# Performance work log

Hardware: AMD Instinct MI355X
Metric: run time of the kernel (lower is better)

Reference implementation:

```python
import jax, jax.numpy as jnp
from jax import lax
import numpy as np

V, E, H, L, B, ML, T = 32000, 512, 512, 2, 64, 64, 32


def setup_inputs() -> dict:
    key = jax.random.key(0)
    ks = jax.random.split(key, 16)
    s = 0.05
    return {
        "current_input": jax.random.randint(ks[0], (B,), 0, V),
        "h0": jax.random.normal(ks[1], (L, B, H), jnp.float32),
        "c0": jax.random.normal(ks[2], (L, B, H), jnp.float32),
        "encoder_output": jax.random.normal(ks[3], (ML, B, H), jnp.float32),
        "gtruth": jax.random.randint(ks[4], (T, B), 0, V),
        "length": T,
        "emb": s * jax.random.normal(ks[5], (V, E), jnp.float32),
        "attn_W": s * jax.random.normal(ks[6], (ML, E + H), jnp.float32),
        "attn_out_W": s * jax.random.normal(ks[7], (E, E + H), jnp.float32),
        "lstm_Wi": s * jax.random.normal(ks[8], (L, 4 * H, E), jnp.float32),
        "lstm_Wh": s * jax.random.normal(ks[9], (L, 4 * H, H), jnp.float32),
        "lstm_bi": s * jax.random.normal(ks[10], (L, 4 * H), jnp.float32),
        "lstm_bh": s * jax.random.normal(ks[11], (L, 4 * H), jnp.float32),
        "gen_W": s * jax.random.normal(ks[12], (V, H), jnp.float32),
        "gen_b": s * jax.random.normal(ks[13], (V,), jnp.float32),
    }


def _lstm_cell(x, h, c, Wi, Wh, bi, bh):
    # PyTorch gate order: i, f, g, o
    g = x @ Wi.T + h @ Wh.T + bi + bh  # [B, 4H]
    i, f, gg, o = jnp.split(g, 4, axis=-1)
    c_new = jax.nn.sigmoid(f) * c + jax.nn.sigmoid(i) * jnp.tanh(gg)
    h_new = jax.nn.sigmoid(o) * jnp.tanh(c_new)
    return h_new, c_new


def reference(current_input, h0, c0, encoder_output, gtruth, length,
              emb, attn_W, attn_out_W, lstm_Wi, lstm_Wh, lstm_bi, lstm_bh,
              gen_W, gen_b):
    n_layers = h0.shape[0]

    def step_fn(carry, tok):
        h, c = carry  # each [L, B, H]
        emb_t = emb[tok]                                   # [B, E]
        attn_in = jnp.concatenate([emb_t, h[-1]], axis=1)  # [B, E+H]
        a = jax.nn.softmax(attn_in @ attn_W.T, axis=1)     # [B, ML]
        ctx = jnp.einsum('bl,lbh->bh', a, encoder_output)  # [B, H]
        rnn_in = jax.nn.relu(
            jnp.concatenate([emb_t, ctx], axis=1) @ attn_out_W.T)  # [B, E]
        x = rnn_in
        hs, cs = [], []
        for l in range(n_layers):
            hn, cn = _lstm_cell(x, h[l], c[l], lstm_Wi[l], lstm_Wh[l],
                                lstm_bi[l], lstm_bh[l])
            hs.append(hn)
            cs.append(cn)
            x = hn
        scores = x @ gen_W.T + gen_b  # [B, V]
        return (jnp.stack(hs), jnp.stack(cs)), scores

    # teacher forcing: step t consumes current_input at t=0, gtruth[t-1] after
    tokens = jnp.concatenate([current_input[None], gtruth[:-1]], axis=0)  # [T, B]
    (h_fin, c_fin), outputs = lax.scan(step_fn, (h0, c0), tokens)
    return outputs, h_fin, c_fin
```

## Files before the change

kernel.cpp:

```cpp
#include <hip/hip_runtime.h>
#include <hip/hip_bf16.h>

typedef __bf16 bf16_t;
typedef bf16_t bf16x8 __attribute__((ext_vector_type(8)));
typedef bf16_t bf16x4 __attribute__((ext_vector_type(4)));
typedef float f32x4 __attribute__((ext_vector_type(4)));

#define MFMA(a, b, c) __builtin_amdgcn_mfma_f32_16x16x32_bf16((a), (b), (c), 0, 0, 0)

__device__ __forceinline__ float sigm(float x) { return 1.f / (1.f + __expf(-x)); }
__device__ __forceinline__ float tanh_f(float x) { return 1.f - 2.f / (__expf(2.f * x) + 1.f); }

__device__ __forceinline__ bf16x8 cvt8(const float* p) {
    f32x4 a = *(const f32x4*)p, b = *(const f32x4*)(p + 4);
    bf16x8 v;
#pragma unroll
    for (int i = 0; i < 4; ++i) { v[i] = (bf16_t)a[i]; v[4 + i] = (bf16_t)b[i]; }
    return v;
}

__device__ __forceinline__ void gbar(int* cnt, int target) {
    __syncthreads();
    if (threadIdx.x == 0) {
        __threadfence();
        __hip_atomic_fetch_add(cnt, 1, __ATOMIC_RELEASE, __HIP_MEMORY_SCOPE_AGENT);
        while (__hip_atomic_load(cnt, __ATOMIC_ACQUIRE, __HIP_MEMORY_SCOPE_AGENT) < target)
            __builtin_amdgcn_s_sleep(2);
        __threadfence();
    }
    __syncthreads();
}

__global__ void k_cvt(const float* __restrict__ src, bf16_t* __restrict__ dst, int n) {
    int i = (blockIdx.x * 256 + threadIdx.x) * 8;
    if (i < n) *(bf16x8*)(dst + i) = cvt8(src + i);
}

__global__ void k_init(const float* __restrict__ h0, const float* __restrict__ c0,
                       const float* __restrict__ bi, const float* __restrict__ bh,
                       float* __restrict__ c_f32, bf16_t* __restrict__ h_bf,
                       float* __restrict__ bsum, int* __restrict__ bar) {
    int idx = blockIdx.x * 256 + threadIdx.x;
    if (idx < 65536) { c_f32[idx] = c0[idx]; h_bf[idx] = (bf16_t)h0[idx]; }
    if (idx < 4096) bsum[idx] = bi[idx] + bh[idx];
    if (idx == 0) *bar = 0;
}

__global__ __launch_bounds__(256) void k_pre(const float* __restrict__ emb,
                                             const int* __restrict__ cur, const int* __restrict__ gt,
                                             const bf16_t* __restrict__ Bm, int ldb, int koff,
                                             float* __restrict__ out, int ldo) {
    int tid = threadIdx.x, lane = tid & 63, w = tid >> 6;
    int m = lane & 15, q = lane >> 4;
    int mrow = blockIdx.x * 64 + w * 16 + m;
    int tok = (mrow < 64) ? cur[mrow] : gt[mrow - 64];
    const float* arow = emb + (size_t)tok * 512;
    int n0 = blockIdx.y * 64;
    const bf16_t* brow0 = Bm + (size_t)(n0 + m) * ldb + koff;
    f32x4 acc[4] = {};
    for (int ks = 0; ks < 16; ++ks) {
        int kc = ks * 32 + q * 8;
        bf16x8 a = cvt8(arow + kc);
#pragma unroll
        for (int nt = 0; nt < 4; ++nt) {
            bf16x8 b = *(const bf16x8*)(brow0 + (size_t)nt * 16 * ldb + kc);
            acc[nt] = MFMA(a, b, acc[nt]);
        }
    }
    int rbase = blockIdx.x * 64 + w * 16 + q * 4;
#pragma unroll
    for (int nt = 0; nt < 4; ++nt)
#pragma unroll
        for (int i = 0; i < 4; ++i)
            out[(size_t)(rbase + i) * ldo + n0 + nt * 16 + m] = acc[nt][i];
}

__device__ __forceinline__ void lstm_phase(int wg, int tid,
                                           const bf16_t* __restrict__ x,
                                           const bf16_t* __restrict__ hprev,
                                           const bf16_t* __restrict__ Wi,
                                           const bf16_t* __restrict__ Wh,
                                           const float* __restrict__ bsum,
                                           float* __restrict__ c,
                                           bf16_t* __restrict__ hout,
                                           bf16_t* __restrict__ xs_out) {
    int lane = tid & 63, w = tid >> 6;
    int m = lane & 15, q = lane >> 4;
    int j0 = wg * 16;
    const bf16_t* ax = x + (size_t)(w * 16 + m) * 512;
    const bf16_t* ah = hprev + (size_t)(w * 16 + m) * 512;
    f32x4 acc[4] = {};
    for (int ks = 0; ks < 16; ++ks) {
        int kc = ks * 32 + q * 8;
        bf16x8 a = *(const bf16x8*)(ax + kc);
#pragma unroll
        for (int g = 0; g < 4; ++g) {
            const bf16_t* bp = Wi + (size_t)(g * 512 + j0 + m) * 512 + kc;
            acc[g] = MFMA(a, *(const bf16x8*)bp, acc[g]);
        }
    }
    for (int ks = 0; ks < 16; ++ks) {
        int kc = ks * 32 + q * 8;
        bf16x8 a = *(const bf16x8*)(ah + kc);
#pragma unroll
        for (int g = 0; g < 4; ++g) {
            const bf16_t* bp = Wh + (size_t)(g * 512 + j0 + m) * 512 + kc;
            acc[g] = MFMA(a, *(const bf16x8*)bp, acc[g]);
        }
    }
    int j = j0 + m;
    float bs0 = bsum[j], bs1 = bsum[512 + j], bs2 = bsum[1024 + j], bs3 = bsum[1536 + j];
#pragma unroll
    for (int i = 0; i < 4; ++i) {
        int b = w * 16 + q * 4 + i;
        float ig = acc[0][i] + bs0;
        float fg = acc[1][i] + bs1;
        float gg = acc[2][i] + bs2;
        float og = acc[3][i] + bs3;
        size_t off = (size_t)b * 512 + j;
        float co = c[off];
        float cn = sigm(fg) * co + sigm(ig) * tanh_f(gg);
        float hn = sigm(og) * tanh_f(cn);
        c[off] = cn;
        hout[off] = (bf16_t)hn;
        if (xs_out) xs_out[off] = (bf16_t)hn;
    }
}

__global__ __launch_bounds__(256) void k_loop(const bf16_t* __restrict__ attn_W_bf,
                                              const bf16_t* __restrict__ attn_out_W_bf,
                                              const float* __restrict__ enc,
                                              const float* __restrict__ pre_s,
                                              const float* __restrict__ pre_r,
                                              const bf16_t* __restrict__ Wi_bf,
                                              const bf16_t* __restrict__ Wh_bf,
                                              const float* __restrict__ bsum,
                                              float* __restrict__ c_f32,
                                              bf16_t* __restrict__ h_bf,
                                              bf16_t* __restrict__ ctx_bf,
                                              bf16_t* __restrict__ rnn_bf,
                                              bf16_t* __restrict__ xs,
                                              int* __restrict__ bar) {
    __shared__ float s_p[2][64];
    int tid = threadIdx.x, lane = tid & 63, w = tid >> 6;
    int m = lane & 15, q = lane >> 4;
    int wg = blockIdx.x;
    int b0 = wg * 2;
    int bt = 0;

    for (int t = 0; t < 32; ++t) {
        int p = t & 1;
        const bf16_t* h1p = h_bf + (size_t)p * 65536;
        const bf16_t* h2p = h1p + 32768;
        bf16_t* h1n = h_bf + (size_t)(p ^ 1) * 65536;
        bf16_t* h2n = h1n + 32768;

        {
            const bf16_t* aptr = h2p + (size_t)(b0 + (m & 1)) * 512;
            const bf16_t* bptr = attn_W_bf + (size_t)(w * 16 + m) * 1024 + 512;
            f32x4 acc = {};
            for (int ks = 0; ks < 16; ++ks) {
                int kc = ks * 32 + q * 8;
                acc = MFMA(*(const bf16x8*)(aptr + kc), *(const bf16x8*)(bptr + kc), acc);
            }
            if (q == 0) {
#pragma unroll
                for (int i = 0; i < 2; ++i)
                    s_p[i][w * 16 + m] =
                        acc[i] + pre_s[((size_t)t * 64 + b0 + i) * 64 + w * 16 + m];
            }
        }
        __syncthreads();
        if (tid < 128) {
            int r = tid >> 6, l = tid & 63;
            float v = s_p[r][l];
            float mx = v;
#pragma unroll
            for (int off = 32; off; off >>= 1) mx = fmaxf(mx, __shfl_xor(mx, off));
            float e = __expf(v - mx);
            float s = e;
#pragma unroll
            for (int off = 32; off; off >>= 1) s += __shfl_xor(s, off);
            s_p[r][l] = e / s;
        }
        __syncthreads();
        {
            int r = tid >> 7, c0 = (tid & 127) * 4;
            int b = b0 + r;
            f32x4 acc = {};
            const float* ebase = enc + (size_t)b * 512 + c0;
            for (int l = 0; l < 64; ++l) {
                float a = s_p[r][l];
                f32x4 e = *(const f32x4*)(ebase + (size_t)l * 32768);
#pragma unroll
                for (int i = 0; i < 4; ++i) acc[i] += a * e[i];
            }
            bf16x4 cv;
#pragma unroll
            for (int i = 0; i < 4; ++i) cv[i] = (bf16_t)acc[i];
            *(bf16x4*)(ctx_bf + (size_t)b * 512 + c0) = cv;
        }
        bt += 32; gbar(bar, bt);

        {
            int j0 = wg * 16;
            const bf16_t* actx = ctx_bf + (size_t)(w * 16 + m) * 512;
            const bf16_t* bptr = attn_out_W_bf + (size_t)(j0 + m) * 1024 + 512;
            f32x4 acc = {};
            for (int ks = 0; ks < 16; ++ks) {
                int kc = ks * 32 + q * 8;
                acc = MFMA(*(const bf16x8*)(actx + kc), *(const bf16x8*)(bptr + kc), acc);
            }
            int jj = j0 + m;
#pragma unroll
            for (int i = 0; i < 4; ++i) {
                int b = w * 16 + q * 4 + i;
                float v = acc[i] + pre_r[((size_t)t * 64 + b) * 512 + jj];
                rnn_bf[(size_t)b * 512 + jj] = (bf16_t)fmaxf(v, 0.f);
            }
        }
        bt += 32; gbar(bar, bt);

        lstm_phase(wg, tid, rnn_bf, h1p, Wi_bf, Wh_bf, bsum, c_f32, h1n, nullptr);
        bt += 32; gbar(bar, bt);

        lstm_phase(wg, tid, h1n, h2p, Wi_bf + 1048576, Wh_bf + 1048576, bsum + 2048,
                   c_f32 + 32768, h2n, xs + (size_t)t * 32768);
        bt += 32; gbar(bar, bt);
    }
}

__global__ __launch_bounds__(256) void k_gen(const bf16_t* __restrict__ xs,
                                             const bf16_t* __restrict__ gen_W,
                                             const float* __restrict__ gen_b,
                                             float* __restrict__ out) {
    __shared__ bf16_t sA[64 * 256];
    int tid = threadIdx.x, lane = tid & 63, w = tid >> 6;
    int m = lane & 15, q4 = lane >> 4;
    int m0 = blockIdx.x * 64, n0 = blockIdx.y * 256;
    f32x4 acc[4][4] = {};
    for (int ko = 0; ko < 2; ++ko) {
        __syncthreads();
#pragma unroll
        for (int it = 0; it < 8; ++it) {
            int idx = it * 256 + tid;
            int mr = idx >> 5, qc = idx & 31;
            bf16x8 v = *(const bf16x8*)(xs + (size_t)(m0 + mr) * 512 + ko * 256 + qc * 8);
            *(bf16x8*)(&sA[(mr * 32 + (qc ^ (mr & 7))) * 8]) = v;
        }
        __syncthreads();
        const bf16_t* bbase = gen_W + (size_t)(n0 + w * 64 + m) * 512 + ko * 256;
        for (int ks = 0; ks < 8; ++ks) {
            bf16x8 af[4];
#pragma unroll
            for (int mt = 0; mt < 4; ++mt) {
                int r = mt * 16 + m, chunk = ks * 4 + q4;
                af[mt] = *(const bf16x8*)(&sA[(r * 32 + (chunk ^ (r & 7))) * 8]);
            }
            int kc = ks * 32 + q4 * 8;
#pragma unroll
            for (int nt = 0; nt < 4; ++nt) {
                bf16x8 bfrag = *(const bf16x8*)(bbase + (size_t)nt * 16 * 512 + kc);
#pragma unroll
                for (int mt = 0; mt < 4; ++mt) acc[mt][nt] = MFMA(af[mt], bfrag, acc[mt][nt]);
            }
        }
    }
#pragma unroll
    for (int nt = 0; nt < 4; ++nt) {
        int col = n0 + w * 64 + nt * 16 + m;
        float bias = gen_b[col];
#pragma unroll
        for (int mt = 0; mt < 4; ++mt)
#pragma unroll
            for (int i = 0; i < 4; ++i) {
                int r = m0 + mt * 16 + q4 * 4 + i;
                out[(size_t)r * 32000 + col] = acc[mt][nt][i] + bias;
            }
    }
}

__global__ void k_tail(const bf16_t* __restrict__ h_bf0, const float* __restrict__ c_f32,
                       float* __restrict__ out) {
    int idx = blockIdx.x * 256 + threadIdx.x;
    if (idx < 65536) {
        out[65536000 + idx] = (float)h_bf0[idx];
        out[65601536 + idx] = c_f32[idx];
    }
}

extern "C" void kernel_launch(void* const* d_in, const int* in_sizes, int n_in,
                              void* d_out, int out_size, void* d_ws, size_t ws_size,
                              hipStream_t stream) {
    const int* cur = (const int*)d_in[0];
    const float* h0 = (const float*)d_in[1];
    const float* c0 = (const float*)d_in[2];
    const float* enc = (const float*)d_in[3];
    const int* gt = (const int*)d_in[4];
    const float* emb = (const float*)d_in[6];
    const float* attn_W = (const float*)d_in[7];
    const float* attn_out_W = (const float*)d_in[8];
    const float* Wi = (const float*)d_in[9];
    const float* Wh = (const float*)d_in[10];
    const float* bi = (const float*)d_in[11];
    const float* bh = (const float*)d_in[12];
    const float* gen_W = (const float*)d_in[13];
    const float* gen_b = (const float*)d_in[14];
    float* out = (float*)d_out;

    char* ws = (char*)d_ws;
    float* c_f32 = (float*)(ws + 0);
    bf16_t* h_bf = (bf16_t*)(ws + 262144);
    float* bsum = (float*)(ws + 524288);
    float* pre_s = (float*)(ws + 540672);
    float* pre_r = (float*)(ws + 1064960);
    bf16_t* rnn_bf = (bf16_t*)(ws + 5259264);
    bf16_t* xs = (bf16_t*)(ws + 5324800);
    bf16_t* attn_W_bf = (bf16_t*)(ws + 7421952);
    bf16_t* attn_out_W_bf = (bf16_t*)(ws + 7553024);
    bf16_t* Wi_bf = (bf16_t*)(ws + 8601600);
    bf16_t* Wh_bf = (bf16_t*)(ws + 12795904);
    bf16_t* gen_W_bf = (bf16_t*)(ws + 16990208);
    bf16_t* ctx_bf = (bf16_t*)(ws + 49758208);
    int* bar = (int*)(ws + 49823744);

    k_cvt<<<32, 256, 0, stream>>>(attn_W, attn_W_bf, 65536);
    k_cvt<<<256, 256, 0, stream>>>(attn_out_W, attn_out_W_bf, 524288);
    k_cvt<<<1024, 256, 0, stream>>>(Wi, Wi_bf, 2097152);
    k_cvt<<<1024, 256, 0, stream>>>(Wh, Wh_bf, 2097152);
    k_cvt<<<8000, 256, 0, stream>>>(gen_W, gen_W_bf, 16384000);
    k_init<<<256, 256, 0, stream>>>(h0, c0, bi, bh, c_f32, h_bf, bsum, bar);
    k_pre<<<dim3(32, 1), 256, 0, stream>>>(emb, cur, gt, attn_W_bf, 1024, 0, pre_s, 64);
    k_pre<<<dim3(32, 8), 256, 0, stream>>>(emb, cur, gt, attn_out_W_bf, 1024, 0, pre_r, 512);

    k_loop<<<32, 256, 0, stream>>>(attn_W_bf, attn_out_W_bf, enc, pre_s, pre_r,
                                   Wi_bf, Wh_bf, bsum, c_f32, h_bf, ctx_bf, rnn_bf, xs, bar);

    k_gen<<<dim3(32, 125), 256, 0, stream>>>(xs, gen_W_bf, gen_b, out);
    k_tail<<<256, 256, 0, stream>>>(h_bf, c_f32, out);
}
```

Before: 3.567 ms.

## Relax grid barrier fences using per-step buffers and agent-scope atomic stores

The grid barrier drops its thread fences and release/acquire ordering and uses relaxed atomics instead. Cross-block data (h, ctx, rnn) is now written with relaxed agent-scope atomic stores into per-timestep buffers rather than ping-pong buffers, so values are never overwritten and stale-cache reuse is avoided. This is meant to cut the cost of the many barriers per step. In exchange it uses more workspace, and correctness now depends on relaxed stores becoming visible without fences, which is a memory-ordering risk. c_f32 is still written with plain stores.

```diff
diff --git a/kernel.cpp b/kernel.cpp
--- a/kernel.cpp
+++ b/kernel.cpp
@@ -19,14 +19,21 @@
     return v;
 }
 
+__device__ __forceinline__ void st4c(bf16_t* p, bf16x4 v) {
+    __hip_atomic_store((unsigned long long*)p, __builtin_bit_cast(unsigned long long, v),
+                       __ATOMIC_RELAXED, __HIP_MEMORY_SCOPE_AGENT);
+}
+__device__ __forceinline__ void st1c(bf16_t* p, bf16_t v) {
+    __hip_atomic_store((unsigned short*)p, __builtin_bit_cast(unsigned short, v),
+                       __ATOMIC_RELAXED, __HIP_MEMORY_SCOPE_AGENT);
+}
+
 __device__ __forceinline__ void gbar(int* cnt, int target) {
     __syncthreads();
     if (threadIdx.x == 0) {
-        __threadfence();
-        __hip_atomic_fetch_add(cnt, 1, __ATOMIC_RELEASE, __HIP_MEMORY_SCOPE_AGENT);
-        while (__hip_atomic_load(cnt, __ATOMIC_ACQUIRE, __HIP_MEMORY_SCOPE_AGENT) < target)
+        __hip_atomic_fetch_add(cnt, 1, __ATOMIC_RELAXED, __HIP_MEMORY_SCOPE_AGENT);
+        while (__hip_atomic_load(cnt, __ATOMIC_RELAXED, __HIP_MEMORY_SCOPE_AGENT) < target)
             __builtin_amdgcn_s_sleep(2);
-        __threadfence();
     }
     __syncthreads();
 }
@@ -38,10 +45,12 @@
 
 __global__ void k_init(const float* __restrict__ h0, const float* __restrict__ c0,
                        const float* __restrict__ bi, const float* __restrict__ bh,
-                       float* __restrict__ c_f32, bf16_t* __restrict__ h_bf,
-                       float* __restrict__ bsum, int* __restrict__ bar) {
+                       float* __restrict__ c_f32, bf16_t* __restrict__ h1_0,
+                       bf16_t* __restrict__ h2_0, float* __restrict__ bsum,
+                       int* __restrict__ bar) {
     int idx = blockIdx.x * 256 + threadIdx.x;
-    if (idx < 65536) { c_f32[idx] = c0[idx]; h_bf[idx] = (bf16_t)h0[idx]; }
+    if (idx < 65536) c_f32[idx] = c0[idx];
+    if (idx < 32768) { h1_0[idx] = (bf16_t)h0[idx]; h2_0[idx] = (bf16_t)h0[32768 + idx]; }
     if (idx < 4096) bsum[idx] = bi[idx] + bh[idx];
     if (idx == 0) *bar = 0;
 }
@@ -122,7 +131,7 @@
         float cn = sigm(fg) * co + sigm(ig) * tanh_f(gg);
         float hn = sigm(og) * tanh_f(cn);
         c[off] = cn;
-        hout[off] = (bf16_t)hn;
+        st1c(hout + off, (bf16_t)hn);
         if (xs_out) xs_out[off] = (bf16_t)hn;
     }
 }
@@ -136,9 +145,10 @@
                                               const bf16_t* __restrict__ Wh_bf,
                                               const float* __restrict__ bsum,
                                               float* __restrict__ c_f32,
-                                              bf16_t* __restrict__ h_bf,
-                                              bf16_t* __restrict__ ctx_bf,
-                                              bf16_t* __restrict__ rnn_bf,
+                                              bf16_t* __restrict__ h1_buf,
+                                              bf16_t* __restrict__ h2_buf,
+                                              bf16_t* __restrict__ ctx_buf,
+                                              bf16_t* __restrict__ rnn_buf,
                                               bf16_t* __restrict__ xs,
                                               int* __restrict__ bar) {
     __shared__ float s_p[2][64];
@@ -149,11 +159,12 @@
     int bt = 0;
 
     for (int t = 0; t < 32; ++t) {
-        int p = t & 1;
-        const bf16_t* h1p = h_bf + (size_t)p * 65536;
-        const bf16_t* h2p = h1p + 32768;
-        bf16_t* h1n = h_bf + (size_t)(p ^ 1) * 65536;
-        bf16_t* h2n = h1n + 32768;
+        const bf16_t* h1p = h1_buf + (size_t)t * 32768;
+        const bf16_t* h2p = h2_buf + (size_t)t * 32768;
+        bf16_t* h1n = h1_buf + (size_t)(t + 1) * 32768;
+        bf16_t* h2n = h2_buf + (size_t)(t + 1) * 32768;
+        bf16_t* ctx_t = ctx_buf + (size_t)t * 32768;
+        const bf16_t* rnn_t = rnn_buf + (size_t)t * 32768;
 
         {
             const bf16_t* aptr = h2p + (size_t)(b0 + (m & 1)) * 512;
@@ -198,13 +209,13 @@
             bf16x4 cv;
 #pragma unroll
             for (int i = 0; i < 4; ++i) cv[i] = (bf16_t)acc[i];
-            *(bf16x4*)(ctx_bf + (size_t)b * 512 + c0) = cv;
+            st4c(ctx_t + (size_t)b * 512 + c0, cv);
         }
         bt += 32; gbar(bar, bt);
 
         {
             int j0 = wg * 16;
-            const bf16_t* actx = ctx_bf + (size_t)(w * 16 + m) * 512;
+            const bf16_t* actx = ctx_t + (size_t)(w * 16 + m) * 512;
             const bf16_t* bptr = attn_out_W_bf + (size_t)(j0 + m) * 1024 + 512;
             f32x4 acc = {};
             for (int ks = 0; ks < 16; ++ks) {
@@ -216,12 +227,12 @@
             for (int i = 0; i < 4; ++i) {
                 int b = w * 16 + q * 4 + i;
                 float v = acc[i] + pre_r[((size_t)t * 64 + b) * 512 + jj];
-                rnn_bf[(size_t)b * 512 + jj] = (bf16_t)fmaxf(v, 0.f);
+                st1c((bf16_t*)rnn_t + (size_t)b * 512 + jj, (bf16_t)fmaxf(v, 0.f));
             }
         }
         bt += 32; gbar(bar, bt);
 
-        lstm_phase(wg, tid, rnn_bf, h1p, Wi_bf, Wh_bf, bsum, c_f32, h1n, nullptr);
+        lstm_phase(wg, tid, rnn_t, h1p, Wi_bf, Wh_bf, bsum, c_f32, h1n, nullptr);
         bt += 32; gbar(bar, bt);
 
         lstm_phase(wg, tid, h1n, h2p, Wi_bf + 1048576, Wh_bf + 1048576, bsum + 2048,
@@ -280,11 +291,12 @@
     }
 }
 
-__global__ void k_tail(const bf16_t* __restrict__ h_bf0, const float* __restrict__ c_f32,
-                       float* __restrict__ out) {
+__global__ void k_tail(const bf16_t* __restrict__ h1f, const bf16_t* __restrict__ h2f,
+                       const float* __restrict__ c_f32, float* __restrict__ out) {
     int idx = blockIdx.x * 256 + threadIdx.x;
     if (idx < 65536) {
-        out[65536000 + idx] = (float)h_bf0[idx];
+        float hv = (idx < 32768) ? (float)h1f[idx] : (float)h2f[idx - 32768];
+        out[65536000 + idx] = hv;
         out[65601536 + idx] = c_f32[idx];
     }
 }
@@ -310,32 +322,34 @@
 
     char* ws = (char*)d_ws;
     float* c_f32 = (float*)(ws + 0);
-    bf16_t* h_bf = (bf16_t*)(ws + 262144);
     float* bsum = (float*)(ws + 524288);
     float* pre_s = (float*)(ws + 540672);
     float* pre_r = (float*)(ws + 1064960);
-    bf16_t* rnn_bf = (bf16_t*)(ws + 5259264);
     bf16_t* xs = (bf16_t*)(ws + 5324800);
     bf16_t* attn_W_bf = (bf16_t*)(ws + 7421952);
     bf16_t* attn_out_W_bf = (bf16_t*)(ws + 7553024);
     bf16_t* Wi_bf = (bf16_t*)(ws + 8601600);
     bf16_t* Wh_bf = (bf16_t*)(ws + 12795904);
     bf16_t* gen_W_bf = (bf16_t*)(ws + 16990208);
-    bf16_t* ctx_bf = (bf16_t*)(ws + 49758208);
-    int* bar = (int*)(ws + 49823744);
+    bf16_t* h1_buf = (bf16_t*)(ws + 49758208);
+    bf16_t* h2_buf = (bf16_t*)(ws + 51920896);
+    bf16_t* ctx_buf = (bf16_t*)(ws + 54083584);
+    bf16_t* rnn_buf = (bf16_t*)(ws + 56180736);
+    int* bar = (int*)(ws + 58277888);
 
     k_cvt<<<32, 256, 0, stream>>>(attn_W, attn_W_bf, 65536);
     k_cvt<<<256, 256, 0, stream>>>(attn_out_W, attn_out_W_bf, 524288);
     k_cvt<<<1024, 256, 0, stream>>>(Wi, Wi_bf, 2097152);
     k_cvt<<<1024, 256, 0, stream>>>(Wh, Wh_bf, 2097152);
     k_cvt<<<8000, 256, 0, stream>>>(gen_W, gen_W_bf, 16384000);
-    k_init<<<256, 256, 0, stream>>>(h0, c0, bi, bh, c_f32, h_bf, bsum, bar);
+    k_init<<<256, 256, 0, stream>>>(h0, c0, bi, bh, c_f32, h1_buf, h2_buf, bsum, bar);
     k_pre<<<dim3(32, 1), 256, 0, stream>>>(emb, cur, gt, attn_W_bf, 1024, 0, pre_s, 64);
     k_pre<<<dim3(32, 8), 256, 0, stream>>>(emb, cur, gt, attn_out_W_bf, 1024, 0, pre_r, 512);
 
     k_loop<<<32, 256, 0, stream>>>(attn_W_bf, attn_out_W_bf, enc, pre_s, pre_r,
-                                   Wi_bf, Wh_bf, bsum, c_f32, h_bf, ctx_bf, rnn_bf, xs, bar);
+                                   Wi_bf, Wh_bf, bsum, c_f32, h1_buf, h2_buf,
+                                   ctx_buf, rnn_buf, xs, bar);
 
     k_gen<<<dim3(32, 125), 256, 0, stream>>>(xs, gen_W_bf, gen_b, out);
-    k_tail<<<256, 256, 0, stream>>>(h_bf, c_f32, out);
-}
+    k_tail<<<256, 256, 0, stream>>>(h1_buf + 32 * 32768, h2_buf + 32 * 32768, c_f32, out);
+}
```

Result: no change. 3.574 ms (+0.2%).
